# Performance work log

Measured on AMD Instinct MI355X. Metric: run time of the kernel, lower is better.

Reference implementation:

```python
import jax, jax.numpy as jnp
import numpy as np

C = 256
HEADS = 8
HD = C // HEADS
EPS = 1e-5


def _layernorm(x, g, b):
    mu = jnp.mean(x, axis=-1, keepdims=True)
    var = jnp.var(x, axis=-1, keepdims=True)
    return (x - mu) * jax.lax.rsqrt(var + EPS) * g + b


def setup_inputs() -> dict:
    key = jax.random.key(0)
    ks = jax.random.split(key, 16)
    s = 0.02
    return {
        "x": jax.random.normal(ks[0], (1, C, 64, 64), jnp.float32),
        "bn_gamma": 1.0 + s * jax.random.normal(ks[1], (C,), jnp.float32),
        "bn_beta": s * jax.random.normal(ks[2], (C,), jnp.float32),
        "bn_mean": s * jax.random.normal(ks[3], (C,), jnp.float32),
        "bn_var": jnp.ones((C,), jnp.float32),
        "w_in": s * jax.random.normal(ks[4], (C, C), jnp.float32),
        "b_in": jnp.zeros((C,), jnp.float32),
        "ln1_g": jnp.ones((C,), jnp.float32),
        "ln1_b": jnp.zeros((C,), jnp.float32),
        "w_qkv": s * jax.random.normal(ks[5], (3 * C, C), jnp.float32),
        "b_qkv": jnp.zeros((3 * C,), jnp.float32),
        "w_ap": s * jax.random.normal(ks[6], (C, C), jnp.float32),
        "b_ap": jnp.zeros((C,), jnp.float32),
        "ln2_g": jnp.ones((C,), jnp.float32),
        "ln2_b": jnp.zeros((C,), jnp.float32),
        "w_ff1": s * jax.random.normal(ks[7], (4 * C, C), jnp.float32),
        "b_ff1": jnp.zeros((4 * C,), jnp.float32),
        "w_ff2": s * jax.random.normal(ks[8], (C, 4 * C), jnp.float32),
        "b_ff2": jnp.zeros((C,), jnp.float32),
        "w_out": s * jax.random.normal(ks[9], (C, C), jnp.float32),
        "b_out": jnp.zeros((C,), jnp.float32),
    }


def reference(x, bn_gamma, bn_beta, bn_mean, bn_var, w_in, b_in,
              ln1_g, ln1_b, w_qkv, b_qkv, w_ap, b_ap,
              ln2_g, ln2_b, w_ff1, b_ff1, w_ff2, b_ff2, w_out, b_out):
    b, c, h, w = x.shape
    t = h * w
    x_in = x
    # BatchNorm2d (eval mode: running stats)
    xn = (x - bn_mean[None, :, None, None]) * jax.lax.rsqrt(bn_var + EPS)[None, :, None, None]
    xn = xn * bn_gamma[None, :, None, None] + bn_beta[None, :, None, None]
    # proj_in 1x1 conv -> tokens [b, t, c]
    tok = xn.reshape(b, c, t).transpose(0, 2, 1)
    tok = tok @ w_in.T + b_in
    # transformer block (depth=1)
    y = _layernorm(tok, ln1_g, ln1_b)  # norm1
    qkv = y @ w_qkv.T + b_qkv  # [b, t, 3c], channel split (3, H, hd)
    qkv = qkv.reshape(b, t, 3, HEADS, HD)
    q = qkv[:, :, 0].transpose(0, 2, 1, 3)  # [b, H, t, hd]
    k = qkv[:, :, 1].transpose(0, 2, 1, 3)
    v = qkv[:, :, 2].transpose(0, 2, 1, 3)
    scale = HD ** (-0.5)
    attn = jax.nn.softmax(jnp.einsum('bhqd,bhkd->bhqk', q, k) * scale, axis=-1)
    o = jnp.einsum('bhqk,bhkd->bhqd', attn, v)  # [b, H, t, hd]
    o = o.transpose(0, 2, 1, 3).reshape(b, t, c)  # channels ordered (H, hd)
    o = o @ w_ap.T + b_ap  # attn proj 1x1
    attn_out = o + y  # VanillaAttention residual adds its (normed) input
    tok = tok + attn_out
    # FFN
    z = _layernorm(tok, ln2_g, ln2_b)
    z = jax.nn.gelu(z @ w_ff1.T + b_ff1, approximate=False)
    tok = tok + (z @ w_ff2.T + b_ff2)
    # back to image, proj_out 1x1, outer residual
    x4 = tok.transpose(0, 2, 1).reshape(b, c, h, w)
    out = jnp.einsum('oc,bchw->bohw', w_out, x4) + b_out[None, :, None, None]
    return out + x_in
```

## Files before the change

### kernel.cpp

```cpp
#include <hip/hip_runtime.h>
#include <math.h>

#define T_TOK 4096
#define C_DIM 256
#define EPSF  1e-5f
#define SC_QL (0.17677669529663687f * 1.4426950408889634f)

typedef short  bf16x8  __attribute__((ext_vector_type(8)));
typedef float  f32x4   __attribute__((ext_vector_type(4)));
typedef ushort ushort8 __attribute__((ext_vector_type(8)));
typedef unsigned uint4v __attribute__((ext_vector_type(4)));
typedef unsigned uint2v __attribute__((ext_vector_type(2)));

__device__ __forceinline__ short f2bf(float f) {
    unsigned u = __builtin_bit_cast(unsigned, f);
    unsigned r = (u + 0x7FFFu + ((u >> 16) & 1u)) >> 16;
    return (short)r;
}
__device__ __forceinline__ float bf2f(ushort u) {
    return __builtin_bit_cast(float, ((unsigned)u) << 16);
}
__device__ __forceinline__ unsigned pk_bf16(float a, float b) {
    const unsigned ua = __builtin_bit_cast(unsigned, a) + 0x8000u;
    const unsigned ub = __builtin_bit_cast(unsigned, b) + 0x8000u;
    return __builtin_amdgcn_perm(ub, ua, 0x07060302u);
}
__device__ __forceinline__ unsigned cvtpk_bf16(float a, float b) {
    unsigned r;
    asm("v_cvt_pk_bf16_f32 %0, %1, %2" : "=v"(r) : "v"(a), "v"(b));
    return r;
}
__device__ __forceinline__ void plswap32(unsigned &a, unsigned &b) {
    asm("v_permlane32_swap_b32 %0, %1" : "+v"(a), "+v"(b));
}
__device__ __forceinline__ void plswap16(unsigned &a, unsigned &b) {
    asm("v_permlane16_swap_b32 %0, %1" : "+v"(a), "+v"(b));
}
template <int CTRL>
__device__ __forceinline__ float dppf(float x) {
    return __builtin_bit_cast(float,
        __builtin_amdgcn_mov_dpp(__builtin_bit_cast(int, x), CTRL, 0xF, 0xF, true));
}
__device__ __forceinline__ float rowsum16(float x) {
    x += dppf<0xB1>(x);
    x += dppf<0x4E>(x);
    x += dppf<0x141>(x);
    x += dppf<0x140>(x);
    return x;
}
#define MFMA16(a, b, c) __builtin_amdgcn_mfma_f32_16x16x32_bf16(a, b, c, 0, 0, 0)

__global__ __launch_bounds__(256) void prep_kernel(
    const float* __restrict__ w_in, const float* __restrict__ w_qkv,
    const float* __restrict__ w_ap, const float* __restrict__ w_ff1,
    const float* __restrict__ w_ff2, const float* __restrict__ w_out,
    const float* __restrict__ b_qkv, ushort* __restrict__ wbuf,
    float* __restrict__ bqs,
    const float* __restrict__ x, const float* __restrict__ gamma,
    const float* __restrict__ beta, const float* __restrict__ mean,
    const float* __restrict__ var, ushort* __restrict__ tin)
{
    __shared__ float tile[32][33];
    if (blockIdx.x < 896) {
        const int gid = blockIdx.x * 256 + threadIdx.x;
        const int e0 = gid * 4;
        const float* src; int off; float sc = 1.f;
        if (e0 < 65536)       { src = w_in;  off = e0; }
        else if (e0 < 262144) { src = w_qkv; off = e0 - 65536; if (off < 65536) sc = SC_QL; }
        else if (e0 < 327680) { src = w_ap;  off = e0 - 262144; }
        else if (e0 < 589824) { src = w_ff1; off = e0 - 327680; }
        else if (e0 < 851968) { src = w_ff2; off = e0 - 589824; }
        else                  { src = w_out; off = e0 - 851968; }
        const float4 v = *(const float4*)(src + off);
        ushort4 o;
        o.x = (ushort)f2bf(v.x * sc); o.y = (ushort)f2bf(v.y * sc);
        o.z = (ushort)f2bf(v.z * sc); o.w = (ushort)f2bf(v.w * sc);
        *(ushort4*)(wbuf + e0) = o;
        if (gid < 192) {
            const float s2 = (gid < 64) ? SC_QL : 1.f;
            float4 b = ((const float4*)b_qkv)[gid];
            b.x *= s2; b.y *= s2; b.z *= s2; b.w *= s2;
            ((float4*)bqs)[gid] = b;
        }
    } else {
        const int bidx = blockIdx.x - 896;
        const int t0 = (bidx & 127) * 32, c0 = (bidx >> 7) * 32;
        const int tx = threadIdx.x & 31, ty = threadIdx.x >> 5;
#pragma unroll
        for (int i = 0; i < 32; i += 8) {
            const int c = c0 + ty + i;
            const float a = rsqrtf(var[c] + EPSF) * gamma[c];
            const float d = beta[c] - mean[c] * a;
            tile[ty + i][tx] = x[c * T_TOK + t0 + tx] * a + d;
        }
        __syncthreads();
#pragma unroll
        for (int i = 0; i < 32; i += 8) {
            const int t = t0 + ty + i;
            tin[t * C_DIM + c0 + tx] = (ushort)f2bf(tile[tx][ty + i]);
        }
    }
}

__global__ __launch_bounds__(1024) void fused_pre(
    const ushort* __restrict__ tin, const ushort* __restrict__ wb_in,
    const float* __restrict__ b_in, const float* __restrict__ ln1_g,
    const float* __restrict__ ln1_b, const ushort* __restrict__ wb_qkv,
    const float* __restrict__ bqs, float* __restrict__ tok0,
    float* __restrict__ yout, ushort* __restrict__ qkvb)
{
    __shared__ ushort Atile[16 * 264];
    __shared__ ushort Ytile[16 * 264];
    __shared__ float  red[16][16][2];
    const int t0 = blockIdx.x * 16;
    const int tid = threadIdx.x, wv = tid >> 6, lane = tid & 63;
    const int c = lane & 15, g = lane >> 4;

    {
        const int r = tid >> 6, c0 = (tid & 63) * 4;
        *(ushort4*)&Atile[r * 264 + c0] = *(const ushort4*)(tin + (size_t)(t0 + r) * 256 + c0);
    }
    __syncthreads();

    f32x4 accp = {};
#pragma unroll
    for (int kc = 0; kc < 8; ++kc) {
        const bf16x8 af = *(const bf16x8*)&Atile[c * 264 + kc * 32 + g * 8];
        const bf16x8 bfv = *(const bf16x8*)(wb_in +
            (size_t)(wv * 16 + c) * 256 + kc * 32 + g * 8);
        accp = MFMA16(af, bfv, accp);
    }
    const int colp = wv * 16 + c;
    {
        const float bb = b_in[colp];
        float vs[4], s1[4], s2[4];
#pragma unroll
        for (int rr = 0; rr < 4; ++rr) {
            const float v = accp[rr] + bb;
            vs[rr] = v; s1[rr] = v; s2[rr] = v * v;
            tok0[(size_t)(t0 + 4 * g + rr) * 256 + colp] = v;
        }
#pragma unroll
        for (int rr = 0; rr < 4; ++rr) { s1[rr] = rowsum16(s1[rr]); s2[rr] = rowsum16(s2[rr]); }
        if (c == 0) {
#pragma unroll
            for (int rr = 0; rr < 4; ++rr) {
                red[wv][4 * g + rr][0] = s1[rr];
                red[wv][4 * g + rr][1] = s2[rr];
            }
        }
        __syncthreads();
        if (tid < 32) {
            const int row = tid >> 1, j = tid & 1;
            float s = 0.f;
#pragma unroll
            for (int w = 0; w < 16; ++w) s += red[w][row][j];
            red[0][row][j] = s;
        }
        __syncthreads();
        const float gg = ln1_g[colp], lb = ln1_b[colp];
#pragma unroll
        for (int rr = 0; rr < 4; ++rr) {
            const int row = 4 * g + rr;
            const float mu = red[0][row][0] * (1.0f / 256.0f);
            const float var = red[0][row][1] * (1.0f / 256.0f) - mu * mu;
            const float rs = rsqrtf(var + EPSF);
            const float yv = (vs[rr] - mu) * rs * gg + lb;
            yout[(size_t)(t0 + row) * 256 + colp] = yv;
            Ytile[row * 264 + colp] = (ushort)f2bf(yv);
        }
    }
    __syncthreads();

    f32x4 accq[3] = {};
#pragma unroll
    for (int kc = 0; kc < 8; ++kc) {
        const bf16x8 af = *(const bf16x8*)&Ytile[c * 264 + kc * 32 + g * 8];
#pragma unroll
        for (int nf = 0; nf < 3; ++nf) {
            const bf16x8 bfv = *(const bf16x8*)(wb_qkv +
                (size_t)(wv * 48 + nf * 16 + c) * 256 + kc * 32 + g * 8);
            accq[nf] = MFMA16(af, bfv, accq[nf]);
        }
    }
#pragma unroll
    for (int nf = 0; nf < 3; ++nf) {
        const int col = wv * 48 + nf * 16 + c;
        const float bb = bqs[col];
#pragma unroll
        for (int rr = 0; rr < 4; ++rr)
            qkvb[(size_t)(t0 + 4 * g + rr) * 768 + col] = (ushort)f2bf(accq[nf][rr] + bb);
    }
}

#define KS   40
#define VTS  72

__global__ __launch_bounds__(256) void attn_mfma(
    const ushort* __restrict__ qkv, ushort* __restrict__ o1,
    ushort* __restrict__ o2, ushort* __restrict__ o3,
    ushort* __restrict__ o4, float* __restrict__ lpart)
{
    const int h    = blockIdx.y;
    const int q0   = blockIdx.x << 6;
    const int qrt  = blockIdx.z;
    const int tid  = threadIdx.x;
    const int wv   = tid >> 6, lane = tid & 63;
    const int c    = lane & 15, g = lane >> 4;

    __shared__ ushort Ks[2][64 * KS];
    __shared__ ushort Vt[2][32 * VTS];

    const bf16x8 qf = *(const bf16x8*)(qkv + (size_t)(q0 + wv * 16 + c) * 768 + h * 32 + g * 8);

    bf16x8 ones;
#pragma unroll
    for (int i = 0; i < 8; ++i) ones[i] = (short)0x3F80;

    f32x4 oacc0 = {0.f, 0.f, 0.f, 0.f};
    f32x4 oacc1 = {0.f, 0.f, 0.f, 0.f};
    f32x4 oaccl = {0.f, 0.f, 0.f, 0.f};

    const int kr = wv * 16 + c, kc = g * 8;
    const int vp = tid & 31, vd = (tid >> 5) * 4;
    const ushort* kbase = qkv + 256 + h * 32;
    const ushort* vbase = qkv + 512 + h * 32;

    const int kt0 = qrt * 16, kt1 = kt0 + 16;

    {
        const ushort8 kv = *(const ushort8*)(kbase + ((size_t)kt0 * 64 + kr) * 768 + kc);
        const uint2v va = *(const uint2v*)(vbase + ((size_t)kt0 * 64 + 2 * vp) * 768 + vd);
        const uint2v vb = *(const uint2v*)(vbase + ((size_t)kt0 * 64 + 2 * vp + 1) * 768 + vd);
        *(ushort8*)&Ks[0][kr * KS + kc] = kv;
        unsigned* vtp = (unsigned*)&Vt[0][0];
        vtp[(vd + 0) * (VTS / 2) + vp] = __builtin_amdgcn_perm(vb.x, va.x, 0x05040100u);
        vtp[(vd + 1) * (VTS / 2) + vp] = __builtin_amdgcn_perm(vb.x, va.x, 0x07060302u);
        vtp[(vd + 2) * (VTS / 2) + vp] = __builtin_amdgcn_perm(vb.y, va.y, 0x05040100u);
        vtp[(vd + 3) * (VTS / 2) + vp] = __builtin_amdgcn_perm(vb.y, va.y, 0x07060302u);
    }
    ushort8 kpre = *(const ushort8*)(kbase + ((size_t)(kt0 + 1) * 64 + kr) * 768 + kc);
    uint2v vpre0 = *(const uint2v*)(vbase + ((size_t)(kt0 + 1) * 64 + 2 * vp) * 768 + vd);
    uint2v vpre1 = *(const uint2v*)(vbase + ((size_t)(kt0 + 1) * 64 + 2 * vp + 1) * 768 + vd);
    __syncthreads();

    int p = 0;
    for (int kt = kt0; kt < kt1; ++kt) {
        const ushort* ks = &Ks[p][0];
        const ushort* vt = &Vt[p][0];
        const bf16x8 k0 = *(const bf16x8*)&ks[(0 * 16 + c) * KS + g * 8];
        const bf16x8 k1 = *(const bf16x8*)&ks[(1 * 16 + c) * KS + g * 8];
        const bf16x8 k2 = *(const bf16x8*)&ks[(2 * 16 + c) * KS + g * 8];
        const bf16x8 k3 = *(const bf16x8*)&ks[(3 * 16 + c) * KS + g * 8];

        if (kt + 1 < kt1) {
            *(ushort8*)&Ks[p ^ 1][kr * KS + kc] = kpre;
            unsigned* vtp = (unsigned*)&Vt[p ^ 1][0];
            vtp[(vd + 0) * (VTS / 2) + vp] = __builtin_amdgcn_perm(vpre1.x, vpre0.x, 0x05040100u);
            vtp[(vd + 1) * (VTS / 2) + vp] = __builtin_amdgcn_perm(vpre1.x, vpre0.x, 0x07060302u);
            vtp[(vd + 2) * (VTS / 2) + vp] = __builtin_amdgcn_perm(vpre1.y, vpre0.y, 0x05040100u);
            vtp[(vd + 3) * (VTS / 2) + vp] = __builtin_amdgcn_perm(vpre1.y, vpre0.y, 0x07060302u);
            if (kt + 2 < kt1) {
                const size_t t2 = (size_t)(kt + 2) * 64;
                kpre  = *(const ushort8*)(kbase + (t2 + kr) * 768 + kc);
                vpre0 = *(const uint2v*)(vbase + (t2 + 2 * vp) * 768 + vd);
                vpre1 = *(const uint2v*)(vbase + (t2 + 2 * vp + 1) * 768 + vd);
            }
        }

        const f32x4 zz = {0.f, 0.f, 0.f, 0.f};
        const f32x4 s0 = MFMA16(k0, qf, zz);
        const f32x4 s1 = MFMA16(k1, qf, zz);
        const f32x4 s2 = MFMA16(k2, qf, zz);
        const f32x4 s3 = MFMA16(k3, qf, zz);

        unsigned w00 = cvtpk_bf16(__builtin_amdgcn_exp2f(s0[0]), __builtin_amdgcn_exp2f(s0[1]));
        unsigned w01 = cvtpk_bf16(__builtin_amdgcn_exp2f(s0[2]), __builtin_amdgcn_exp2f(s0[3]));
        unsigned w10 = cvtpk_bf16(__builtin_amdgcn_exp2f(s1[0]), __builtin_amdgcn_exp2f(s1[1]));
        unsigned w11 = cvtpk_bf16(__builtin_amdgcn_exp2f(s1[2]), __builtin_amdgcn_exp2f(s1[3]));
        unsigned w20 = cvtpk_bf16(__builtin_amdgcn_exp2f(s2[0]), __builtin_amdgcn_exp2f(s2[1]));
        unsigned w21 = cvtpk_bf16(__builtin_amdgcn_exp2f(s2[2]), __builtin_amdgcn_exp2f(s2[3]));
        unsigned w30 = cvtpk_bf16(__builtin_amdgcn_exp2f(s3[0]), __builtin_amdgcn_exp2f(s3[1]));
        unsigned w31 = cvtpk_bf16(__builtin_amdgcn_exp2f(s3[2]), __builtin_amdgcn_exp2f(s3[3]));

        plswap32(w00, w10); plswap16(w00, w10);
        plswap32(w01, w11); plswap16(w01, w11);
        plswap32(w20, w30); plswap16(w20, w30);
        plswap32(w21, w31); plswap16(w21, w31);
        const uint4v u0 = {w00, w01, w10, w11};
        const uint4v u1 = {w20, w21, w30, w31};
        const bf16x8 pa0 = __builtin_bit_cast(bf16x8, u0);
        const bf16x8 pa1 = __builtin_bit_cast(bf16x8, u1);

        {
            const bf16x8 va0 = *(const bf16x8*)&vt[(c)      * VTS + 0 * 32 + g * 8];
            const bf16x8 vb0 = *(const bf16x8*)&vt[(16 + c) * VTS + 0 * 32 + g * 8];
            oacc0 = MFMA16(pa0, va0, oacc0);
            oacc1 = MFMA16(pa0, vb0, oacc1);
            oaccl = MFMA16(pa0, ones, oaccl);
            const bf16x8 va1 = *(const bf16x8*)&vt[(c)      * VTS + 1 * 32 + g * 8];
            const bf16x8 vb1 = *(const bf16x8*)&vt[(16 + c) * VTS + 1 * 32 + g * 8];
            oacc0 = MFMA16(pa1, va1, oacc0);
            oacc1 = MFMA16(pa1, vb1, oacc1);
            oaccl = MFMA16(pa1, ones, oaccl);
        }
        p ^= 1;
        __syncthreads();
    }

    {
        ushort* ob = (qrt & 2) ? ((qrt & 1) ? o4 : o3) : ((qrt & 1) ? o2 : o1);
        ushort* op = ob + (size_t)(q0 + wv * 16) * 256 + h * 32;
#pragma unroll
        for (int rr = 0; rr < 4; ++rr) {
            op[(4 * g + rr) * 256 + c]      = (ushort)f2bf(oacc0[rr]);
            op[(4 * g + rr) * 256 + 16 + c] = (ushort)f2bf(oacc1[rr]);
        }
        if (c == 0) {
#pragma unroll
            for (int rr = 0; rr < 4; ++rr)
                lpart[(size_t)(q0 + wv * 16 + 4 * g + rr) * 32 + qrt * 8 + h] = oaccl[rr];
        }
    }
}

__global__ __launch_bounds__(1024) void fused_tail(
    const ushort* __restrict__ o1, const ushort* __restrict__ o2,
    const ushort* __restrict__ o3, const ushort* __restrict__ o4,
    const float* __restrict__ lpart, const ushort* __restrict__ wb_ap,
    const float* __restrict__ b_ap, const float* __restrict__ yin,
    const float* __restrict__ tok0, const float* __restrict__ ln2_g,
    const float* __restrict__ ln2_b, const ushort* __restrict__ wb_ff1,
    const float* __restrict__ b_ff1, const ushort* __restrict__ wb_ff2,
    const float* __restrict__ b_ff2, const ushort* __restrict__ wb_out,
    const float* __restrict__ b_out, const float* __restrict__ x,
    float* __restrict__ out)
{
    __shared__ ushort Otile[16 * 264];
    __shared__ ushort Ztile[16 * 264];
    __shared__ ushort Zbig[16 * 1032];
    __shared__ ushort T2tile[16 * 264];
    __shared__ float  red[16][16][2];
    const int t0 = blockIdx.x * 16;
    const int tid = threadIdx.x, wv = tid >> 6, lane = tid & 63;
    const int c = lane & 15, g = lane >> 4;

    {
        const int r = tid >> 6, c0 = (tid & 63) * 4;
        const int h = (tid & 63) >> 3;
        const float* lp = lpart + (size_t)(t0 + r) * 32;
        const float inv = 1.0f / (lp[h] + lp[8 + h] + lp[16 + h] + lp[24 + h]);
        const size_t idx = (size_t)(t0 + r) * 256 + c0;
        const ushort4 a = *(const ushort4*)(o1 + idx);
        const ushort4 b = *(const ushort4*)(o2 + idx);
        const ushort4 d = *(const ushort4*)(o3 + idx);
        const ushort4 e = *(const ushort4*)(o4 + idx);
        unsigned w[2];
        w[0] = pk_bf16((bf2f(a.x) + bf2f(b.x) + bf2f(d.x) + bf2f(e.x)) * inv,
                       (bf2f(a.y) + bf2f(b.y) + bf2f(d.y) + bf2f(e.y)) * inv);
        w[1] = pk_bf16((bf2f(a.z) + bf2f(b.z) + bf2f(d.z) + bf2f(e.z)) * inv,
                       (bf2f(a.w) + bf2f(b.w) + bf2f(d.w) + bf2f(e.w)) * inv);
        *(ushort4*)&Otile[r * 264 + c0] = *(ushort4*)w;
    }
    __syncthreads();

    f32x4 accp = {};
#pragma unroll
    for (int kc = 0; kc < 8; ++kc) {
        const bf16x8 af = *(const bf16x8*)&Otile[c * 264 + kc * 32 + g * 8];
        const bf16x8 bfv = *(const bf16x8*)(wb_ap +
            (size_t)(wv * 16 + c) * 256 + kc * 32 + g * 8);
        accp = MFMA16(af, bfv, accp);
    }
    const int colp = wv * 16 + c;
    float vsave[4];
    {
        const float bb = b_ap[colp];
        float s1[4], s2[4];
#pragma unroll
        for (int rr = 0; rr < 4; ++rr) {
            const size_t idx = (size_t)(t0 + 4 * g + rr) * 256 + colp;
            const float v = accp[rr] + bb + yin[idx] + tok0[idx];
            vsave[rr] = v; s1[rr] = v; s2[rr] = v * v;
        }
#pragma unroll
        for (int rr = 0; rr < 4; ++rr) { s1[rr] = rowsum16(s1[rr]); s2[rr] = rowsum16(s2[rr]); }
        if (c == 0) {
#pragma unroll
            for (int rr = 0; rr < 4; ++rr) {
                red[wv][4 * g + rr][0] = s1[rr];
                red[wv][4 * g + rr][1] = s2[rr];
            }
        }
        __syncthreads();
        if (tid < 32) {
            const int row = tid >> 1, j = tid & 1;
            float s = 0.f;
#pragma unroll
            for (int w = 0; w < 16; ++w) s += red[w][row][j];
            red[0][row][j] = s;
        }
        __syncthreads();
        const float gg = ln2_g[colp], lb = ln2_b[colp];
#pragma unroll
        for (int rr = 0; rr < 4; ++rr) {
            const int row = 4 * g + rr;
            const float mu = red[0][row][0] * (1.0f / 256.0f);
            const float var = red[0][row][1] * (1.0f / 256.0f) - mu * mu;
            const float rs = rsqrtf(var + EPSF);
            const float zv = (vsave[rr] - mu) * rs * gg + lb;
            Ztile[row * 264 + colp] = (ushort)f2bf(zv);
        }
    }
    __syncthreads();

    {
        f32x4 accf[4] = {};
#pragma unroll
        for (int kc = 0; kc < 8; ++kc) {
            const bf16x8 af = *(const bf16x8*)&Ztile[c * 264 + kc * 32 + g * 8];
#pragma unroll
            for (int nf = 0; nf < 4; ++nf) {
                const bf16x8 bfv = *(const bf16x8*)(wb_ff1 +
                    (size_t)(wv * 64 + nf * 16 + c) * 256 + kc * 32 + g * 8);
                accf[nf] = MFMA16(af, bfv, accf[nf]);
            }
        }
#pragma unroll
        for (int nf = 0; nf < 4; ++nf) {
            const int col = wv * 64 + nf * 16 + c;
            const float bb = b_ff1[col];
#pragma unroll
            for (int rr = 0; rr < 4; ++rr) {
                float v = accf[nf][rr] + bb;
                v = 0.5f * v * (1.0f + erff(v * 0.70710678118654752f));
                Zbig[(4 * g + rr) * 1032 + col] = (ushort)f2bf(v);
            }
        }
    }
    __syncthreads();

    {
        f32x4 accf = {};
#pragma unroll
        for (int kc = 0; kc < 32; ++kc) {
            const bf16x8 af = *(const bf16x8*)&Zbig[c * 1032 + kc * 32 + g * 8];
            const bf16x8 bfv = *(const bf16x8*)(wb_ff2 +
                (size_t)(wv * 16 + c) * 1024 + kc * 32 + g * 8);
            accf = MFMA16(af, bfv, accf);
        }
        const float bb = b_ff2[colp];
#pragma unroll
        for (int rr = 0; rr < 4; ++rr) {
            const float v = accf[rr] + bb + vsave[rr];
            T2tile[(4 * g + rr) * 264 + colp] = (ushort)f2bf(v);
        }
    }
    __syncthreads();

    f32x4 acco = {};
#pragma unroll
    for (int kc = 0; kc < 8; ++kc) {
        const bf16x8 bfr = *(const bf16x8*)&T2tile[c * 264 + kc * 32 + g * 8];
        const bf16x8 afr = *(const bf16x8*)(wb_out +
            (size_t)(wv * 16 + c) * 256 + kc * 32 + g * 8);
        acco = MFMA16(afr, bfr, acco);
    }
#pragma unroll
    for (int rr = 0; rr < 4; ++rr) {
        const int och = wv * 16 + 4 * g + rr;
        const size_t idx = (size_t)och * T_TOK + t0 + c;
        out[idx] = acco[rr] + b_out[och] + x[idx];
    }
}

extern "C" void kernel_launch(void* const* d_in, const int* in_sizes, int n_in,
                              void* d_out, int out_size, void* d_ws, size_t ws_size,
                              hipStream_t stream)
{
    const float* x     = (const float*)d_in[0];
    const float* bn_g  = (const float*)d_in[1];
    const float* bn_b  = (const float*)d_in[2];
    const float* bn_m  = (const float*)d_in[3];
    const float* bn_v  = (const float*)d_in[4];
    const float* w_in  = (const float*)d_in[5];
    const float* b_in  = (const float*)d_in[6];
    const float* ln1_g = (const float*)d_in[7];
    const float* ln1_b = (const float*)d_in[8];
    const float* w_qkv = (const float*)d_in[9];
    const float* b_qkv = (const float*)d_in[10];
    const float* w_ap  = (const float*)d_in[11];
    const float* b_ap  = (const float*)d_in[12];
    const float* ln2_g = (const float*)d_in[13];
    const float* ln2_b = (const float*)d_in[14];
    const float* w_ff1 = (const float*)d_in[15];
    const float* b_ff1 = (const float*)d_in[16];
    const float* w_ff2 = (const float*)d_in[17];
    const float* b_ff2 = (const float*)d_in[18];
    const float* w_out = (const float*)d_in[19];
    const float* b_out = (const float*)d_in[20];
    float* out = (float*)d_out;
    float* ws  = (float*)d_ws;

    const size_t MF = 1u << 20;
    float*  tok0   = ws;
    float*  y      = ws + MF;
    ushort* qkv_bf = (ushort*)(ws + 3 * MF);
    ushort* tin_bf = (ushort*)(ws + 6 * MF + MF / 2);
    ushort* o1p    = tin_bf;
    ushort* o2p    = (ushort*)(ws + 7 * MF);
    ushort* o3p    = (ushort*)(ws + 7 * MF + MF / 2);
    ushort* o4p    = (ushort*)(ws + 8 * MF);
    float*  lpart  = ws + 8 * MF + MF / 2;
    ushort* wbuf   = (ushort*)(ws + 8 * MF + MF / 2 + 131072);
    const ushort* wb_in  = wbuf;
    const ushort* wb_qkv = wbuf + 65536;
    const ushort* wb_ap  = wbuf + 262144;
    const ushort* wb_ff1 = wbuf + 327680;
    const ushort* wb_ff2 = wbuf + 589824;
    const ushort* wb_out = wbuf + 851968;
    float* bqs = (float*)(wbuf + 917504);

    prep_kernel<<<1920, 256, 0, stream>>>(w_in, w_qkv, w_ap, w_ff1, w_ff2, w_out,
                                          b_qkv, wbuf, bqs,
                                          x, bn_g, bn_b, bn_m, bn_v, tin_bf);
    fused_pre<<<256, 1024, 0, stream>>>(tin_bf, wb_in, b_in, ln1_g, ln1_b,
                                        wb_qkv, bqs, tok0, y, qkv_bf);
    attn_mfma<<<dim3(64, 8, 4), 256, 0, stream>>>(qkv_bf, o1p, o2p, o3p, o4p, lpart);
    fused_tail<<<256, 1024, 0, stream>>>(o1p, o2p, o3p, o4p, lpart, wb_ap, b_ap,
                                         y, tok0, ln2_g, ln2_b, wb_ff1, b_ff1,
                                         wb_ff2, b_ff2, wb_out, b_out, x, out);
}
```

Before: 208.1 us.

## Merge y and tok0 into one residual buffer, use fast GELU, remap K loads

The pre kernel now writes a single fp32 buffer holding y plus tok0 instead of two separate buffers, and the tail kernel reads that one buffer. This halves the residual traffic between the kernels. The exact erf GELU is replaced by a sigmoid-style approximation built on exp2 and rcp, which is cheaper but changes numerics slightly. The K-tile load indexing in attention is also remapped so each thread row loads a contiguous chunk, which should improve coalescing.

Result: faster. 200.4 us (-3.7%).

```diff
diff --git a/kernel.cpp b/kernel.cpp
--- a/kernel.cpp
+++ b/kernel.cpp
@@ -47,6 +47,12 @@
     x += dppf<0x141>(x);
     x += dppf<0x140>(x);
     return x;
+}
+__device__ __forceinline__ float gelu_f(float v) {
+    const float u  = v * v;
+    const float w2 = fmaf(u, 0.10294310f, 2.30220800f);
+    const float t  = __builtin_amdgcn_exp2f(v * w2);
+    return v * t * __builtin_amdgcn_rcpf(t + 1.0f);
 }
 #define MFMA16(a, b, c) __builtin_amdgcn_mfma_f32_16x16x32_bf16(a, b, c, 0, 0, 0)
 
@@ -106,8 +112,8 @@
     const ushort* __restrict__ tin, const ushort* __restrict__ wb_in,
     const float* __restrict__ b_in, const float* __restrict__ ln1_g,
     const float* __restrict__ ln1_b, const ushort* __restrict__ wb_qkv,
-    const float* __restrict__ bqs, float* __restrict__ tok0,
-    float* __restrict__ yout, ushort* __restrict__ qkvb)
+    const float* __restrict__ bqs, float* __restrict__ ysum,
+    ushort* __restrict__ qkvb)
 {
     __shared__ ushort Atile[16 * 264];
     __shared__ ushort Ytile[16 * 264];
@@ -138,7 +144,6 @@
         for (int rr = 0; rr < 4; ++rr) {
             const float v = accp[rr] + bb;
             vs[rr] = v; s1[rr] = v; s2[rr] = v * v;
-            tok0[(size_t)(t0 + 4 * g + rr) * 256 + colp] = v;
         }
 #pragma unroll
         for (int rr = 0; rr < 4; ++rr) { s1[rr] = rowsum16(s1[rr]); s2[rr] = rowsum16(s2[rr]); }
@@ -166,7 +171,7 @@
             const float var = red[0][row][1] * (1.0f / 256.0f) - mu * mu;
             const float rs = rsqrtf(var + EPSF);
             const float yv = (vs[rr] - mu) * rs * gg + lb;
-            yout[(size_t)(t0 + row) * 256 + colp] = yv;
+            ysum[(size_t)(t0 + row) * 256 + colp] = yv + vs[rr];
             Ytile[row * 264 + colp] = (ushort)f2bf(yv);
         }
     }
@@ -221,7 +226,7 @@
     f32x4 oacc1 = {0.f, 0.f, 0.f, 0.f};
     f32x4 oaccl = {0.f, 0.f, 0.f, 0.f};
 
-    const int kr = wv * 16 + c, kc = g * 8;
+    const int kr = tid >> 2, kc = (tid & 3) * 8;
     const int vp = tid & 31, vd = (tid >> 5) * 4;
     const ushort* kbase = qkv + 256 + h * 32;
     const ushort* vbase = qkv + 512 + h * 32;
@@ -328,13 +333,12 @@
     const ushort* __restrict__ o1, const ushort* __restrict__ o2,
     const ushort* __restrict__ o3, const ushort* __restrict__ o4,
     const float* __restrict__ lpart, const ushort* __restrict__ wb_ap,
-    const float* __restrict__ b_ap, const float* __restrict__ yin,
-    const float* __restrict__ tok0, const float* __restrict__ ln2_g,
-    const float* __restrict__ ln2_b, const ushort* __restrict__ wb_ff1,
-    const float* __restrict__ b_ff1, const ushort* __restrict__ wb_ff2,
-    const float* __restrict__ b_ff2, const ushort* __restrict__ wb_out,
-    const float* __restrict__ b_out, const float* __restrict__ x,
-    float* __restrict__ out)
+    const float* __restrict__ b_ap, const float* __restrict__ ysum,
+    const float* __restrict__ ln2_g, const float* __restrict__ ln2_b,
+    const ushort* __restrict__ wb_ff1, const float* __restrict__ b_ff1,
+    const ushort* __restrict__ wb_ff2, const float* __restrict__ b_ff2,
+    const ushort* __restrict__ wb_out, const float* __restrict__ b_out,
+    const float* __restrict__ x, float* __restrict__ out)
 {
     __shared__ ushort Otile[16 * 264];
     __shared__ ushort Ztile[16 * 264];
@@ -380,7 +384,7 @@
 #pragma unroll
         for (int rr = 0; rr < 4; ++rr) {
             const size_t idx = (size_t)(t0 + 4 * g + rr) * 256 + colp;
-            const float v = accp[rr] + bb + yin[idx] + tok0[idx];
+            const float v = accp[rr] + bb + ysum[idx];
             vsave[rr] = v; s1[rr] = v; s2[rr] = v * v;
         }
 #pragma unroll
@@ -432,8 +436,7 @@
             const float bb = b_ff1[col];
 #pragma unroll
             for (int rr = 0; rr < 4; ++rr) {
-                float v = accf[nf][rr] + bb;
-                v = 0.5f * v * (1.0f + erff(v * 0.70710678118654752f));
+                const float v = gelu_f(accf[nf][rr] + bb);
                 Zbig[(4 * g + rr) * 1032 + col] = (ushort)f2bf(v);
             }
         }
@@ -503,8 +506,7 @@
     float* ws  = (float*)d_ws;
 
     const size_t MF = 1u << 20;
-    float*  tok0   = ws;
-    float*  y      = ws + MF;
+    float*  ysum   = ws + MF;
     ushort* qkv_bf = (ushort*)(ws + 3 * MF);
     ushort* tin_bf = (ushort*)(ws + 6 * MF + MF / 2);
     ushort* o1p    = tin_bf;
@@ -525,9 +527,9 @@
                                           b_qkv, wbuf, bqs,
                                           x, bn_g, bn_b, bn_m, bn_v, tin_bf);
     fused_pre<<<256, 1024, 0, stream>>>(tin_bf, wb_in, b_in, ln1_g, ln1_b,
-                                        wb_qkv, bqs, tok0, y, qkv_bf);
+                                        wb_qkv, bqs, ysum, qkv_bf);
     attn_mfma<<<dim3(64, 8, 4), 256, 0, stream>>>(qkv_bf, o1p, o2p, o3p, o4p, lpart);
     fused_tail<<<256, 1024, 0, stream>>>(o1p, o2p, o3p, o4p, lpart, wb_ap, b_ap,
-                                         y, tok0, ln2_g, ln2_b, wb_ff1, b_ff1,
+                                         ysum, ln2_g, ln2_b, wb_ff1, b_ff1,
                                          wb_ff2, b_ff2, wb_out, b_out, x, out);
 }
```
